# Kernel optimization log

Measured on AMD Instinct MI355X. Metric: run time of the kernel, lower is better.

Reference implementation:

```python
import jax, jax.numpy as jnp
import numpy as np

N_ENT = 100000
K = 64
D = 500            # emb_dim (complex half-dim); entity embedding is 2*D
R = 237            # num_relations
ATTN = 128
B = 1024
ETA_MAX = 0.5


def setup_inputs() -> dict:
    key = jax.random.key(0)
    ks = jax.random.split(key, 12)
    anchor_ids = jax.random.randint(ks[0], (B,), 0, N_ENT)
    nbr_ent = jax.random.randint(ks[1], (N_ENT, K), 0, N_ENT)
    nbr_rel = jax.random.randint(ks[2], (N_ENT, K), 0, R)
    nbr_dir = jax.random.randint(ks[3], (N_ENT, K), 0, 2).astype(bool)
    nbr_mask = jax.random.randint(ks[4], (N_ENT, K), 0, 2).astype(bool)
    freq = jax.random.uniform(ks[5], (N_ENT,), dtype=jnp.float32) * 1000.0
    entity_embedding = jax.random.normal(ks[6], (N_ENT, 2 * D), dtype=jnp.float32) * 0.1
    # relation phases; get_relation_reim -> (cos(phase), sin(phase))
    rel_phase = jax.random.uniform(ks[7], (R, D), dtype=jnp.float32, minval=-np.pi, maxval=np.pi)
    a_param = jnp.ones((D,), dtype=jnp.float32)
    eta_raw = jnp.float32(-6.0)
    w_raw = jnp.float32(1.0)
    b = jnp.float32(0.0)
    Wq = jax.random.normal(ks[8], (ATTN, 2 * D), dtype=jnp.float32) * 0.01
    Wk = jax.random.normal(ks[9], (ATTN, 2 * D), dtype=jnp.float32) * 0.01
    rel_bias = jax.random.normal(ks[10], (R, 1), dtype=jnp.float32) * 0.01
    dir_bias = jax.random.normal(ks[11], (2, 1), dtype=jnp.float32) * 0.01
    return dict(anchor_ids=anchor_ids, nbr_ent=nbr_ent, nbr_rel=nbr_rel,
                nbr_dir=nbr_dir, nbr_mask=nbr_mask, freq=freq,
                entity_embedding=entity_embedding, rel_phase=rel_phase,
                a_param=a_param, eta_raw=eta_raw, w_raw=w_raw, b=b,
                Wq=Wq, Wk=Wk, rel_bias=rel_bias, dir_bias=dir_bias)


def reference(anchor_ids, nbr_ent, nbr_rel, nbr_dir, nbr_mask, freq,
              entity_embedding, rel_phase, a_param, eta_raw, w_raw, b,
              Wq, Wk, rel_bias, dir_bias):
    # gather per-anchor neighbor tables: [B, K]
    a_ent = nbr_ent[anchor_ids]
    a_rel = nbr_rel[anchor_ids]
    a_dir = nbr_dir[anchor_ids]
    a_msk = nbr_mask[anchor_ids]

    # neighbor entity embeddings [B, K, 2D] -> complex halves [B, K, D]
    e_j = entity_embedding[a_ent]
    re_j, im_j = jnp.split(e_j, 2, axis=-1)

    # RotatE relation rotation (conjugate when dir==True)
    phase = rel_phase[a_rel]                      # [B, K, D]
    re_r = jnp.cos(phase)
    im_r = jnp.sin(phase)
    im_sel = jnp.where(a_dir[..., None], -im_r, im_r)
    re_msg = re_j * re_r - im_j * im_sel
    im_msg = re_j * im_sel + im_j * re_r
    hat = jnp.concatenate([re_msg, im_msg], axis=-1)  # [B, K, 2D]

    e_i = entity_embedding[anchor_ids]            # [B, 2D]

    # small QK attention with relation/direction bias
    q = e_i @ Wq.T                                # [B, A]
    k = hat @ Wk.T                                # [B, K, A]
    scale = max(ATTN ** 0.5, 1e-6)
    logits = jnp.einsum('ba,bka->bk', q, k) / scale
    dir_id = a_dir.astype(jnp.int32)
    logits = logits + rel_bias[a_rel][..., 0] + dir_bias[dir_id][..., 0]
    logits = jnp.where(a_msk, logits, -10000.0)

    has_nbr = jnp.any(a_msk, axis=1)              # [B]
    logits = jnp.where(has_nbr[:, None], logits, 0.0)
    attn = jax.nn.softmax(logits, axis=1)
    attn = jnp.where(has_nbr[:, None], attn, 0.0)

    delta = jnp.einsum('bk,bkd->bd', attn, hat)   # [B, 2D]
    delta = jnp.where(has_nbr[:, None], delta, e_i)

    # frequency-gated interpolation
    logf = jnp.log1p(freq[anchor_ids])
    w = jax.nn.softplus(w_raw)
    eta = ETA_MAX * jax.nn.sigmoid(eta_raw + w * (-logf) + b)
    eta = eta * has_nbr.astype(eta.dtype)

    re_d, im_d = jnp.split(delta, 2, axis=-1)
    re_d = a_param * re_d
    im_d = a_param * im_d
    re_i, im_i = jnp.split(e_i, 2, axis=-1)
    re_out = re_i + eta[:, None] * (re_d - re_i)
    im_out = im_i + eta[:, None] * (im_d - im_i)
    return jnp.concatenate([re_out, im_out], axis=-1)
```

## Files before the change

kernel.cpp:

```cpp
#include <hip/hip_runtime.h>
#include <math.h>

#define KNBR 64
#define DHALF 500
#define TWO_D 1000
#define ATTN_DIM 128
#define ETA_MAX 0.5f

__global__ __launch_bounds__(256) void build_tables(
    const float* __restrict__ P, float* __restrict__ ctab,
    float* __restrict__ stab, int R)
{
    int idx = blockIdx.x * 256 + threadIdx.x;
    if (idx >= R * 512) return;
    int r = idx >> 9, d = idx & 511;
    float c = 0.f, s = 0.f;
    if (d < DHALF) { float ph = P[r * DHALF + d]; sincosf(ph, &s, &c); }
    ctab[idx] = c;
    stab[idx] = s;
}

__global__ __launch_bounds__(256) void build_g2(
    const float* __restrict__ Wq, const float* __restrict__ Wk,
    float* __restrict__ G2)
{
    __shared__ float At[ATTN_DIM][64];
    __shared__ float Bt[ATTN_DIM][64];
    const int t = threadIdx.x;
    const int d1_0 = blockIdx.y * 64, d2_0 = blockIdx.x * 64;
#pragma unroll
    for (int i = 0; i < 32; ++i) {
        int idx = t + 256 * i;
        int a = idx >> 6, c = idx & 63;
        int d1 = d1_0 + c, d2 = d2_0 + c;
        At[a][c] = (d1 < TWO_D) ? Wq[(size_t)a * TWO_D + d1] : 0.f;
        Bt[a][c] = (d2 < TWO_D) ? Wk[(size_t)a * TWO_D + d2] : 0.f;
    }
    __syncthreads();
    const int tx = t & 15, ty = t >> 4;
    float acc[4][4] = {};
    for (int a = 0; a < ATTN_DIM; ++a) {
        float av[4], bv[4];
#pragma unroll
        for (int i = 0; i < 4; ++i) av[i] = At[a][4 * ty + i];
#pragma unroll
        for (int j = 0; j < 4; ++j) bv[j] = Bt[a][4 * tx + j];
#pragma unroll
        for (int i = 0; i < 4; ++i)
#pragma unroll
            for (int j = 0; j < 4; ++j) acc[i][j] += av[i] * bv[j];
    }
    const float inv_scale = 0.0883883476483184f;
#pragma unroll
    for (int i = 0; i < 4; ++i) {
        int d1 = d1_0 + 4 * ty + i;
        if (d1 < TWO_D) {
#pragma unroll
            for (int j = 0; j < 4; ++j) {
                int d2 = d2_0 + 4 * tx + j;
                G2[(size_t)d1 * 1024 + d2] = acc[i][j] * inv_scale;
            }
        }
    }
}

__global__ __launch_bounds__(256) void gemm_M(
    const int* __restrict__ anchor_ids, const float* __restrict__ E,
    const float* __restrict__ G2, float* __restrict__ M, int B)
{
    __shared__ float At[64][33];
    __shared__ float Bt[32][64];
    __shared__ int rows_s[64];
    const int t = threadIdx.x;
    const int bx = blockIdx.x, by = blockIdx.y;
    if (t < 64) { int bb = by * 64 + t; rows_s[t] = (bb < B) ? anchor_ids[bb] : 0; }
    __syncthreads();
    const int tx = t & 15, ty = t >> 4;
    float acc[4][4] = {};
    for (int k0 = 0; k0 < TWO_D; k0 += 32) {
#pragma unroll
        for (int i = 0; i < 8; ++i) {
            int idx = t + 256 * i;
            int r = idx >> 5, c = idx & 31;
            int k = k0 + c;
            At[r][c] = (k < TWO_D) ? E[(size_t)rows_s[r] * TWO_D + k] : 0.f;
        }
#pragma unroll
        for (int i = 0; i < 8; ++i) {
            int idx = t + 256 * i;
            int r = idx >> 6, c = idx & 63;
            int k = k0 + r;
            Bt[r][c] = (k < TWO_D) ? G2[(size_t)k * 1024 + bx * 64 + c] : 0.f;
        }
        __syncthreads();
#pragma unroll
        for (int kk = 0; kk < 32; ++kk) {
            float av[4], bv[4];
#pragma unroll
            for (int i = 0; i < 4; ++i) av[i] = At[4 * ty + i][kk];
#pragma unroll
            for (int j = 0; j < 4; ++j) bv[j] = Bt[kk][4 * tx + j];
#pragma unroll
            for (int i = 0; i < 4; ++i)
#pragma unroll
                for (int j = 0; j < 4; ++j) acc[i][j] += av[i] * bv[j];
        }
        __syncthreads();
    }
#pragma unroll
    for (int i = 0; i < 4; ++i) {
        int b = by * 64 + 4 * ty + i;
        if (b < B) {
#pragma unroll
            for (int j = 0; j < 4; ++j) {
                int d2 = bx * 64 + 4 * tx + j;
                if (d2 < TWO_D) M[(size_t)b * TWO_D + d2] = acc[i][j];
            }
        }
    }
}

struct NbrData {
    float4 re0, re1, im0, im1, c0, c1, s0, s1;
    float rb, ds;
};

__device__ __forceinline__ void load_nbr(
    int j, int lane, const float* __restrict__ E,
    const float* __restrict__ ctab, const float* __restrict__ stab,
    const int* ent_s, const int* rel_s, const float* rb_s, const float* ds_s,
    NbrData& n)
{
    const int ent = ent_s[j];
    const int rel = rel_s[j];
    const float4* er = (const float4*)(E + (size_t)ent * TWO_D);
    const float4* cr = (const float4*)(ctab + (size_t)rel * 512);
    const float4* sr = (const float4*)(stab + (size_t)rel * 512);
    n.re0 = er[lane];
    n.im0 = er[125 + lane];
    n.re1 = make_float4(0.f, 0.f, 0.f, 0.f);
    n.im1 = make_float4(0.f, 0.f, 0.f, 0.f);
    if (lane < 61) {
        n.re1 = er[64 + lane];
        n.im1 = er[189 + lane];
    }
    n.c0 = cr[lane];      n.c1 = cr[64 + lane];
    n.s0 = sr[lane];      n.s1 = sr[64 + lane];
    n.rb = rb_s[j];
    n.ds = ds_s[j];
}

__device__ __forceinline__ void compute_nbr(
    const NbrData& n,
    const float4& mre0, const float4& mre1, const float4& mim0, const float4& mim1,
    float4& are0, float4& are1, float4& aim0, float4& aim1, float& wsum)
{
    const float ds = n.ds;
    float4 hre0, hre1, him0, him1;
    float dot = 0.f;
#define ROT_DOT(F)                                                              \
    {                                                                           \
        float se0 = n.s0.F * ds;                                                \
        hre0.F = n.re0.F * n.c0.F - n.im0.F * se0;                              \
        him0.F = n.re0.F * se0 + n.im0.F * n.c0.F;                              \
        dot += mre0.F * hre0.F + mim0.F * him0.F;                               \
        float se1 = n.s1.F * ds;                                                \
        hre1.F = n.re1.F * n.c1.F - n.im1.F * se1;                              \
        him1.F = n.re1.F * se1 + n.im1.F * n.c1.F;                              \
        dot += mre1.F * hre1.F + mim1.F * him1.F;                               \
    }
    ROT_DOT(x) ROT_DOT(y) ROT_DOT(z) ROT_DOT(w)
#undef ROT_DOT
    dot += __shfl_xor(dot, 32);
    dot += __shfl_xor(dot, 16);
    dot += __shfl_xor(dot, 8);
    dot += __shfl_xor(dot, 4);
    dot += __shfl_xor(dot, 2);
    dot += __shfl_xor(dot, 1);
    const float p = __expf(dot + n.rb);
    wsum += p;
#define ACC(F)                                                                  \
    are0.F += p * hre0.F; are1.F += p * hre1.F;                                 \
    aim0.F += p * him0.F; aim1.F += p * him1.F;
    ACC(x) ACC(y) ACC(z) ACC(w)
#undef ACC
}

__global__ __launch_bounds__(256) void refine(
    const int* __restrict__ anchor_ids,
    const int* __restrict__ nbr_ent,
    const int* __restrict__ nbr_rel,
    const int* __restrict__ nbr_dir,
    const int* __restrict__ nbr_mask,
    const float* __restrict__ freq,
    const float* __restrict__ E,
    const float* __restrict__ ctab,
    const float* __restrict__ stab,
    const float* __restrict__ a_param,
    const float* __restrict__ eta_raw_p,
    const float* __restrict__ w_raw_p,
    const float* __restrict__ b_p,
    const float* __restrict__ rel_bias,
    const float* __restrict__ dir_bias,
    const float* __restrict__ M,
    float* __restrict__ out)
{
    __shared__ float accm[4][TWO_D];
    __shared__ float sum_s[4];
    __shared__ int ent_s[KNBR], rel_s[KNBR];
    __shared__ float rb_s[KNBR], ds_s[KNBR];
    __shared__ int act_n_s;

    const int t = threadIdx.x;
    const int bid = blockIdx.x;
    const int lane = t & 63;
    const int wid = t >> 6;
    const int anchor = anchor_ids[bid];

    if (wid == 0) {
        size_t off = (size_t)anchor * KNBR + lane;
        int msk = nbr_mask[off];
        unsigned long long bal = __ballot(msk != 0);
        if (msk) {
            int rank = __popcll(bal & ((1ull << lane) - 1ull));
            int rel = nbr_rel[off];
            int dirf = nbr_dir[off];
            ent_s[rank] = nbr_ent[off];
            rel_s[rank] = rel;
            ds_s[rank] = dirf ? -1.f : 1.f;
            rb_s[rank] = rel_bias[rel] + dir_bias[dirf ? 1 : 0];
        }
        if (lane == 0) act_n_s = (int)__popcll(bal);
    }
    __syncthreads();
    const int an = act_n_s;

    const float4* mr = (const float4*)(M + (size_t)bid * TWO_D);
    float4 mre0 = mr[lane];
    float4 mim0 = mr[125 + lane];
    float4 mre1 = make_float4(0.f, 0.f, 0.f, 0.f);
    float4 mim1 = make_float4(0.f, 0.f, 0.f, 0.f);
    if (lane < 61) { mre1 = mr[64 + lane]; mim1 = mr[189 + lane]; }

    float4 are0 = make_float4(0.f, 0.f, 0.f, 0.f), are1 = are0, aim0 = are0, aim1 = are0;
    float wsum = 0.f;

    NbrData cur, nxt;
    int j = wid;
    bool have = (j < an);
    if (have) load_nbr(j, lane, E, ctab, stab, ent_s, rel_s, rb_s, ds_s, cur);
    while (have) {
        int jn = j + 4;
        bool haveN = (jn < an);
        if (haveN) load_nbr(jn, lane, E, ctab, stab, ent_s, rel_s, rb_s, ds_s, nxt);
        compute_nbr(cur, mre0, mre1, mim0, mim1, are0, are1, aim0, aim1, wsum);
        cur = nxt;
        j = jn;
        have = haveN;
    }

    if (lane == 0) sum_s[wid] = wsum;
    {
        float4* am = (float4*)(&accm[wid][0]);
        am[lane] = are0;
        am[125 + lane] = aim0;
        if (lane < 61) { am[64 + lane] = are1; am[189 + lane] = aim1; }
    }
    __syncthreads();

    const float S = sum_s[0] + sum_s[1] + sum_s[2] + sum_s[3];
    const float invS = (S > 0.f) ? 1.f / S : 0.f;
    float eta = 0.f;
    if (S > 0.f) {
        float logf_ = log1pf(freq[anchor]);
        float wv = log1pf(__expf(w_raw_p[0]));
        float x = eta_raw_p[0] - wv * logf_ + b_p[0];
        eta = ETA_MAX / (1.f + __expf(-x));
    }

    const float* eirow = E + (size_t)anchor * TWO_D;
#pragma unroll
    for (int c = 0; c < 4; ++c) {
        int dd = t + 256 * c;
        if (dd < TWO_D) {
            float delta = (accm[0][dd] + accm[1][dd] + accm[2][dd] + accm[3][dd]) * invS;
            float ei = eirow[dd];
            float ap = a_param[(dd < DHALF) ? dd : dd - DHALF];
            out[(size_t)bid * TWO_D + dd] = ei + eta * (ap * delta - ei);
        }
    }
}

extern "C" void kernel_launch(void* const* d_in, const int* in_sizes, int n_in,
                              void* d_out, int out_size, void* d_ws, size_t ws_size,
                              hipStream_t stream)
{
    const int*   anchor_ids = (const int*)d_in[0];
    const int*   nbr_ent    = (const int*)d_in[1];
    const int*   nbr_rel    = (const int*)d_in[2];
    const int*   nbr_dir    = (const int*)d_in[3];
    const int*   nbr_mask   = (const int*)d_in[4];
    const float* freq       = (const float*)d_in[5];
    const float* E          = (const float*)d_in[6];
    const float* P          = (const float*)d_in[7];
    const float* a_param    = (const float*)d_in[8];
    const float* eta_raw    = (const float*)d_in[9];
    const float* w_raw      = (const float*)d_in[10];
    const float* b_scalar   = (const float*)d_in[11];
    const float* Wq         = (const float*)d_in[12];
    const float* Wk         = (const float*)d_in[13];
    const float* rel_bias   = (const float*)d_in[14];
    const float* dir_bias   = (const float*)d_in[15];
    float* out = (float*)d_out;

    const int B = in_sizes[0];
    const int R = in_sizes[7] / DHALF;

    auto align256 = [](size_t x) { return (x + 255) & ~(size_t)255; };
    char* ws = (char*)d_ws;
    size_t offM  = 0;
    size_t offG2 = align256(offM + (size_t)B * TWO_D * 4);
    size_t offC  = align256(offG2 + (size_t)TWO_D * 1024 * 4);
    size_t offS  = align256(offC + (size_t)R * 512 * 4);
    float* M    = (float*)(ws + offM);
    float* G2   = (float*)(ws + offG2);
    float* ctab = (float*)(ws + offC);
    float* stab = (float*)(ws + offS);

    build_tables<<<(R * 512 + 255) / 256, 256, 0, stream>>>(P, ctab, stab, R);
    build_g2<<<dim3(16, 16), 256, 0, stream>>>(Wq, Wk, G2);
    gemm_M<<<dim3(16, (B + 63) / 64), 256, 0, stream>>>(anchor_ids, E, G2, M, B);
    refine<<<B, 256, 0, stream>>>(anchor_ids, nbr_ent, nbr_rel, nbr_dir, nbr_mask,
                                  freq, E, ctab, stab, a_param, eta_raw, w_raw,
                                  b_scalar, rel_bias, dir_bias, M, out);
}
```

Before: 733.3 us.

## Vectorize GEMM shared reads and slim refine prefetch to raise occupancy

The M GEMM now stores the A tile transposed (k-major, padded) so each thread reads its four A values with one float4 shared load instead of four scalar ones. The refine kernel now prefetches only the neighbor entity embedding for the next iteration; cos/sin tables are loaded just in time, since they are small and likely cache resident. It also adds a launch-bounds hint of 4 blocks per CU and moves the M row load ahead of the barrier. Together these cut register pressure and shared-memory instructions, at the cost of exposing cos/sin load latency inside the loop and possible register spills under the stricter bound.

```diff
diff --git a/kernel.cpp b/kernel.cpp
--- a/kernel.cpp
+++ b/kernel.cpp
@@ -68,7 +68,7 @@
     const int* __restrict__ anchor_ids, const float* __restrict__ E,
     const float* __restrict__ G2, float* __restrict__ M, int B)
 {
-    __shared__ float At[64][33];
+    __shared__ float At_k[32][65];
     __shared__ float Bt[32][64];
     __shared__ int rows_s[64];
     const int t = threadIdx.x;
@@ -83,7 +83,7 @@
             int idx = t + 256 * i;
             int r = idx >> 5, c = idx & 31;
             int k = k0 + c;
-            At[r][c] = (k < TWO_D) ? E[(size_t)rows_s[r] * TWO_D + k] : 0.f;
+            At_k[c][r] = (k < TWO_D) ? E[(size_t)rows_s[r] * TWO_D + k] : 0.f;
         }
 #pragma unroll
         for (int i = 0; i < 8; ++i) {
@@ -95,15 +95,14 @@
         __syncthreads();
 #pragma unroll
         for (int kk = 0; kk < 32; ++kk) {
-            float av[4], bv[4];
-#pragma unroll
-            for (int i = 0; i < 4; ++i) av[i] = At[4 * ty + i][kk];
-#pragma unroll
-            for (int j = 0; j < 4; ++j) bv[j] = Bt[kk][4 * tx + j];
+            float4 av = *(const float4*)&At_k[kk][4 * ty];
+            float4 bv = *(const float4*)&Bt[kk][4 * tx];
+            const float a4[4] = {av.x, av.y, av.z, av.w};
+            const float b4[4] = {bv.x, bv.y, bv.z, bv.w};
 #pragma unroll
             for (int i = 0; i < 4; ++i)
 #pragma unroll
-                for (int j = 0; j < 4; ++j) acc[i][j] += av[i] * bv[j];
+                for (int j = 0; j < 4; ++j) acc[i][j] += a4[i] * b4[j];
         }
         __syncthreads();
     }
@@ -120,73 +119,7 @@
     }
 }
 
-struct NbrData {
-    float4 re0, re1, im0, im1, c0, c1, s0, s1;
-    float rb, ds;
-};
-
-__device__ __forceinline__ void load_nbr(
-    int j, int lane, const float* __restrict__ E,
-    const float* __restrict__ ctab, const float* __restrict__ stab,
-    const int* ent_s, const int* rel_s, const float* rb_s, const float* ds_s,
-    NbrData& n)
-{
-    const int ent = ent_s[j];
-    const int rel = rel_s[j];
-    const float4* er = (const float4*)(E + (size_t)ent * TWO_D);
-    const float4* cr = (const float4*)(ctab + (size_t)rel * 512);
-    const float4* sr = (const float4*)(stab + (size_t)rel * 512);
-    n.re0 = er[lane];
-    n.im0 = er[125 + lane];
-    n.re1 = make_float4(0.f, 0.f, 0.f, 0.f);
-    n.im1 = make_float4(0.f, 0.f, 0.f, 0.f);
-    if (lane < 61) {
-        n.re1 = er[64 + lane];
-        n.im1 = er[189 + lane];
-    }
-    n.c0 = cr[lane];      n.c1 = cr[64 + lane];
-    n.s0 = sr[lane];      n.s1 = sr[64 + lane];
-    n.rb = rb_s[j];
-    n.ds = ds_s[j];
-}
-
-__device__ __forceinline__ void compute_nbr(
-    const NbrData& n,
-    const float4& mre0, const float4& mre1, const float4& mim0, const float4& mim1,
-    float4& are0, float4& are1, float4& aim0, float4& aim1, float& wsum)
-{
-    const float ds = n.ds;
-    float4 hre0, hre1, him0, him1;
-    float dot = 0.f;
-#define ROT_DOT(F)                                                              \
-    {                                                                           \
-        float se0 = n.s0.F * ds;                                                \
-        hre0.F = n.re0.F * n.c0.F - n.im0.F * se0;                              \
-        him0.F = n.re0.F * se0 + n.im0.F * n.c0.F;                              \
-        dot += mre0.F * hre0.F + mim0.F * him0.F;                               \
-        float se1 = n.s1.F * ds;                                                \
-        hre1.F = n.re1.F * n.c1.F - n.im1.F * se1;                              \
-        him1.F = n.re1.F * se1 + n.im1.F * n.c1.F;                              \
-        dot += mre1.F * hre1.F + mim1.F * him1.F;                               \
-    }
-    ROT_DOT(x) ROT_DOT(y) ROT_DOT(z) ROT_DOT(w)
-#undef ROT_DOT
-    dot += __shfl_xor(dot, 32);
-    dot += __shfl_xor(dot, 16);
-    dot += __shfl_xor(dot, 8);
-    dot += __shfl_xor(dot, 4);
-    dot += __shfl_xor(dot, 2);
-    dot += __shfl_xor(dot, 1);
-    const float p = __expf(dot + n.rb);
-    wsum += p;
-#define ACC(F)                                                                  \
-    are0.F += p * hre0.F; are1.F += p * hre1.F;                                 \
-    aim0.F += p * him0.F; aim1.F += p * him1.F;
-    ACC(x) ACC(y) ACC(z) ACC(w)
-#undef ACC
-}
-
-__global__ __launch_bounds__(256) void refine(
+__global__ __launch_bounds__(256, 4) void refine(
     const int* __restrict__ anchor_ids,
     const int* __restrict__ nbr_ent,
     const int* __restrict__ nbr_rel,
@@ -232,31 +165,76 @@
         }
         if (lane == 0) act_n_s = (int)__popcll(bal);
     }
-    __syncthreads();
-    const int an = act_n_s;
 
     const float4* mr = (const float4*)(M + (size_t)bid * TWO_D);
     float4 mre0 = mr[lane];
     float4 mim0 = mr[125 + lane];
-    float4 mre1 = make_float4(0.f, 0.f, 0.f, 0.f);
-    float4 mim1 = make_float4(0.f, 0.f, 0.f, 0.f);
+    float4 mre1 = make_float4(0.f, 0.f, 0.f, 0.f), mim1 = mre1;
     if (lane < 61) { mre1 = mr[64 + lane]; mim1 = mr[189 + lane]; }
 
-    float4 are0 = make_float4(0.f, 0.f, 0.f, 0.f), are1 = are0, aim0 = are0, aim1 = are0;
+    __syncthreads();
+    const int an = act_n_s;
+
+    float4 are0 = make_float4(0.f, 0.f, 0.f, 0.f);
+    float4 are1 = are0, aim0 = are0, aim1 = are0;
     float wsum = 0.f;
 
-    NbrData cur, nxt;
+    float4 ere0, ere1, eim0, eim1;
+    float4 nre0, nre1, nim0, nim1;
+
     int j = wid;
-    bool have = (j < an);
-    if (have) load_nbr(j, lane, E, ctab, stab, ent_s, rel_s, rb_s, ds_s, cur);
-    while (have) {
-        int jn = j + 4;
-        bool haveN = (jn < an);
-        if (haveN) load_nbr(jn, lane, E, ctab, stab, ent_s, rel_s, rb_s, ds_s, nxt);
-        compute_nbr(cur, mre0, mre1, mim0, mim1, are0, are1, aim0, aim1, wsum);
-        cur = nxt;
-        j = jn;
-        have = haveN;
+    if (j < an) {
+        const float4* er = (const float4*)(E + (size_t)ent_s[j] * TWO_D);
+        ere0 = er[lane];
+        eim0 = er[125 + lane];
+        ere1 = make_float4(0.f, 0.f, 0.f, 0.f); eim1 = ere1;
+        if (lane < 61) { ere1 = er[64 + lane]; eim1 = er[189 + lane]; }
+    }
+    for (; j < an; j += 4) {
+        const int jn = j + 4;
+        if (jn < an) {
+            const float4* er = (const float4*)(E + (size_t)ent_s[jn] * TWO_D);
+            nre0 = er[lane];
+            nim0 = er[125 + lane];
+            nre1 = make_float4(0.f, 0.f, 0.f, 0.f); nim1 = nre1;
+            if (lane < 61) { nre1 = er[64 + lane]; nim1 = er[189 + lane]; }
+        }
+        const int rel = rel_s[j];
+        const float4* cr = (const float4*)(ctab + (size_t)rel * 512);
+        const float4* sr = (const float4*)(stab + (size_t)rel * 512);
+        const float4 c0 = cr[lane], c1 = cr[64 + lane];
+        const float4 s0 = sr[lane], s1 = sr[64 + lane];
+        const float dsg = ds_s[j];
+
+        float4 hre0, hre1, him0, him1;
+        float dot = 0.f;
+#define ROT_DOT(F)                                                          \
+        {                                                                   \
+            float se0 = s0.F * dsg;                                         \
+            hre0.F = ere0.F * c0.F - eim0.F * se0;                          \
+            him0.F = ere0.F * se0 + eim0.F * c0.F;                          \
+            dot += mre0.F * hre0.F + mim0.F * him0.F;                       \
+            float se1 = s1.F * dsg;                                         \
+            hre1.F = ere1.F * c1.F - eim1.F * se1;                          \
+            him1.F = ere1.F * se1 + eim1.F * c1.F;                          \
+            dot += mre1.F * hre1.F + mim1.F * him1.F;                       \
+        }
+        ROT_DOT(x) ROT_DOT(y) ROT_DOT(z) ROT_DOT(w)
+#undef ROT_DOT
+        dot += __shfl_xor(dot, 32);
+        dot += __shfl_xor(dot, 16);
+        dot += __shfl_xor(dot, 8);
+        dot += __shfl_xor(dot, 4);
+        dot += __shfl_xor(dot, 2);
+        dot += __shfl_xor(dot, 1);
+        const float p = __expf(dot + rb_s[j]);
+        wsum += p;
+#define ACC(F)                                                              \
+        are0.F += p * hre0.F; are1.F += p * hre1.F;                         \
+        aim0.F += p * him0.F; aim1.F += p * him1.F;
+        ACC(x) ACC(y) ACC(z) ACC(w)
+#undef ACC
+        ere0 = nre0; ere1 = nre1; eim0 = nim0; eim1 = nim1;
     }
 
     if (lane == 0) sum_s[wid] = wsum;
```

Measured after the change: 731.9 us. About the same (-0.2%).
